# Kernel optimization log

Measured on AMD Instinct MI355X. Metric: run time of the kernel, lower is better.

Reference implementation:

```python
import jax, jax.numpy as jnp
import numpy as np


def setup_inputs() -> dict:
    key = jax.random.key(0)
    B, C, H, W = 16, 96, 128, 128
    x = jax.random.normal(key, (B, C, H, W), dtype=jnp.float32)
    return {"x": x}


def reference(x):
    # CrossScan forward, in_channel_first=True, out_channel_first=True,
    # one_by_one=False, scans=0 (4-directional cross scan).
    B, C, H, W = x.shape
    y0 = x.reshape(B, C, H * W)                       # row-major scan
    y1 = jnp.swapaxes(x, 2, 3).reshape(B, C, H * W)   # column-major scan
    y2 = y0[..., ::-1]                                # reversed row-major
    y3 = y1[..., ::-1]                                # reversed column-major
    return jnp.stack([y0, y1, y2, y3], axis=1)        # [B, 4, C, H*W]
```

## Files before the change

kernel.cpp:

```cpp
#include <hip/hip_runtime.h>


typedef float v4f __attribute__((ext_vector_type(4)));

#define Hh 128
#define Ww 128
#define HWp (Hh * Ww)
#define Cc 96
#define Bb 16
#define TILE 64

__global__ __launch_bounds__(256) void cross_scan_kernel(
    const float* __restrict__ x, float* __restrict__ out) {
  __shared__ float tile[TILE][TILE + 1];

  const int tx = threadIdx.x;
  const int ty = threadIdx.y;
  const int tileId = blockIdx.x;
  const int r0 = (tileId >> 1) * TILE;
  const int c0 = (tileId & 1) * TILE;
  const int plane = blockIdx.y;
  const int b = plane / Cc;
  const int c = plane - b * Cc;

  const float* xp = x + (size_t)plane * HWp;
  float* out0 = out + ((size_t)(b * 4 + 0) * Cc + c) * HWp;
  float* out1 = out + ((size_t)(b * 4 + 1) * Cc + c) * HWp;
  float* out2 = out + ((size_t)(b * 4 + 2) * Cc + c) * HWp;
  float* out3 = out + ((size_t)(b * 4 + 3) * Cc + c) * HWp;

  v4f v[4];
#pragma unroll
  for (int j = 0; j < 4; ++j) {
    const int r = ty + 16 * j;
    v[j] = __builtin_nontemporal_load(
        (const v4f*)(xp + (r0 + r) * Ww + c0 + tx * 4));
  }
#pragma unroll
  for (int j = 0; j < 4; ++j) {
    const int r = ty + 16 * j;
    __builtin_nontemporal_store(
        v[j], (v4f*)(out0 + (r0 + r) * Ww + c0 + tx * 4));
    tile[r][tx * 4 + 0] = v[j][0];
    tile[r][tx * 4 + 1] = v[j][1];
    tile[r][tx * 4 + 2] = v[j][2];
    tile[r][tx * 4 + 3] = v[j][3];
  }
  __syncthreads();

  const int r2b = TILE - r0;
  const int c2b = TILE - c0;
  const int R3b = TILE - c0;
  const int c3b = TILE - r0;

#pragma unroll
  for (int j = 0; j < 4; ++j) {
    const int R = ty + 16 * j;

    v4f t1;
    t1[0] = tile[tx * 4 + 0][R];
    t1[1] = tile[tx * 4 + 1][R];
    t1[2] = tile[tx * 4 + 2][R];
    t1[3] = tile[tx * 4 + 3][R];
    __builtin_nontemporal_store(
        t1, (v4f*)(out1 + (c0 + R) * Hh + r0 + tx * 4));

    const float* Trow = &tile[63 - R][0];
    v4f t2;
    t2[0] = Trow[63 - tx * 4];
    t2[1] = Trow[62 - tx * 4];
    t2[2] = Trow[61 - tx * 4];
    t2[3] = Trow[60 - tx * 4];
    __builtin_nontemporal_store(
        t2, (v4f*)(out2 + (r2b + R) * Ww + c2b + tx * 4));

    v4f t3;
    t3[0] = tile[63 - tx * 4][63 - R];
    t3[1] = tile[62 - tx * 4][63 - R];
    t3[2] = tile[61 - tx * 4][63 - R];
    t3[3] = tile[60 - tx * 4][63 - R];
    __builtin_nontemporal_store(
        t3, (v4f*)(out3 + (R3b + R) * Hh + c3b + tx * 4));
  }
}

extern "C" void kernel_launch(void* const* d_in, const int* in_sizes, int n_in,
                              void* d_out, int out_size, void* d_ws,
                              size_t ws_size, hipStream_t stream) {
  const float* x = (const float*)d_in[0];
  float* out = (float*)d_out;
  dim3 grid(4, Bb * Cc);
  dim3 block(16, 16);
  cross_scan_kernel<<<grid, block, 0, stream>>>(x, out);
}
```

Before: 454.7 us.

## Process whole plane per block with swizzled v4f LDS transpose

```diff
diff --git a/kernel.cpp b/kernel.cpp
--- a/kernel.cpp
+++ b/kernel.cpp
@@ -5,21 +5,16 @@
 
 #define Hh 128
 #define Ww 128
-#define HWp (Hh * Ww)
+#define HWp 16384
 #define Cc 96
 #define Bb 16
-#define TILE 64
 
-__global__ __launch_bounds__(256) void cross_scan_kernel(
+__global__ __launch_bounds__(1024) void cross_scan_kernel(
     const float* __restrict__ x, float* __restrict__ out) {
-  __shared__ float tile[TILE][TILE + 1];
+  __shared__ v4f tile4[128 * 32];
 
-  const int tx = threadIdx.x;
-  const int ty = threadIdx.y;
-  const int tileId = blockIdx.x;
-  const int r0 = (tileId >> 1) * TILE;
-  const int c0 = (tileId & 1) * TILE;
-  const int plane = blockIdx.y;
+  const int T = threadIdx.x;
+  const int plane = blockIdx.x;
   const int b = plane / Cc;
   const int c = plane - b * Cc;
 
@@ -31,56 +26,38 @@
 
   v4f v[4];
 #pragma unroll
-  for (int j = 0; j < 4; ++j) {
-    const int r = ty + 16 * j;
-    v[j] = __builtin_nontemporal_load(
-        (const v4f*)(xp + (r0 + r) * Ww + c0 + tx * 4));
+  for (int p = 0; p < 4; ++p) {
+    const int G = p * 1024 + T;
+    v[p] = __builtin_nontemporal_load((const v4f*)(xp + 4 * G));
   }
 #pragma unroll
-  for (int j = 0; j < 4; ++j) {
-    const int r = ty + 16 * j;
-    __builtin_nontemporal_store(
-        v[j], (v4f*)(out0 + (r0 + r) * Ww + c0 + tx * 4));
-    tile[r][tx * 4 + 0] = v[j][0];
-    tile[r][tx * 4 + 1] = v[j][1];
-    tile[r][tx * 4 + 2] = v[j][2];
-    tile[r][tx * 4 + 3] = v[j][3];
+  for (int p = 0; p < 4; ++p) {
+    const int G = p * 1024 + T;
+    const int r = G >> 5;
+    const int s = G & 31;
+    __builtin_nontemporal_store(v[p], (v4f*)(out0 + 4 * G));
+    v4f rv = {v[p][3], v[p][2], v[p][1], v[p][0]};
+    __builtin_nontemporal_store(rv, (v4f*)(out2 + (16380 - 4 * G)));
+    tile4[r * 32 + (s ^ ((r >> 2) & 7))] = v[p];
   }
   __syncthreads();
 
-  const int r2b = TILE - r0;
-  const int c2b = TILE - c0;
-  const int R3b = TILE - c0;
-  const int c3b = TILE - r0;
-
 #pragma unroll
-  for (int j = 0; j < 4; ++j) {
-    const int R = ty + 16 * j;
-
+  for (int p = 0; p < 4; ++p) {
+    const int Q = p * 1024 + T;
+    const int w = Q >> 5;
+    const int h0 = (Q & 31) * 4;
+    const int sw = w >> 2;
+    const int kw = w & 3;
     v4f t1;
-    t1[0] = tile[tx * 4 + 0][R];
-    t1[1] = tile[tx * 4 + 1][R];
-    t1[2] = tile[tx * 4 + 2][R];
-    t1[3] = tile[tx * 4 + 3][R];
-    __builtin_nontemporal_store(
-        t1, (v4f*)(out1 + (c0 + R) * Hh + r0 + tx * 4));
-
-    const float* Trow = &tile[63 - R][0];
-    v4f t2;
-    t2[0] = Trow[63 - tx * 4];
-    t2[1] = Trow[62 - tx * 4];
-    t2[2] = Trow[61 - tx * 4];
-    t2[3] = Trow[60 - tx * 4];
-    __builtin_nontemporal_store(
-        t2, (v4f*)(out2 + (r2b + R) * Ww + c2b + tx * 4));
-
-    v4f t3;
-    t3[0] = tile[63 - tx * 4][63 - R];
-    t3[1] = tile[62 - tx * 4][63 - R];
-    t3[2] = tile[61 - tx * 4][63 - R];
-    t3[3] = tile[60 - tx * 4][63 - R];
-    __builtin_nontemporal_store(
-        t3, (v4f*)(out3 + (R3b + R) * Hh + c3b + tx * 4));
+#pragma unroll
+    for (int k = 0; k < 4; ++k) {
+      const int r = h0 + k;
+      t1[k] = tile4[r * 32 + (sw ^ ((r >> 2) & 7))][kw];
+    }
+    __builtin_nontemporal_store(t1, (v4f*)(out1 + 4 * Q));
+    v4f rt = {t1[3], t1[2], t1[1], t1[0]};
+    __builtin_nontemporal_store(rt, (v4f*)(out3 + (16380 - 4 * Q)));
   }
 }
 
@@ -89,7 +66,7 @@
                               size_t ws_size, hipStream_t stream) {
   const float* x = (const float*)d_in[0];
   float* out = (float*)d_out;
-  dim3 grid(4, Bb * Cc);
-  dim3 block(16, 16);
+  dim3 grid(Bb * Cc);
+  dim3 block(1024);
   cross_scan_kernel<<<grid, block, 0, stream>>>(x, out);
 }
```

Measured after the change: 459.0 us. No clear change (+1.0%).
